# Performance work log

Hardware: AMD Instinct MI355X
Metric: run time of the kernel (lower is better)

## Reference

```python
import jax, jax.numpy as jnp
import numpy as np

N_NODES = 50000
N_EDGES = 800000
IN_F = 128
OUT_F = 64
ALPHA = 0.2  # LeakyReLU negative slope


def setup_inputs() -> dict:
    key = jax.random.key(0)
    k_h, k_e, k_w, k_b, k_a = jax.random.split(key, 5)
    h = jax.random.normal(k_h, (N_NODES, IN_F), dtype=jnp.float32)
    adj = jax.random.randint(k_e, (2, N_EDGES), 0, N_NODES, dtype=jnp.int64)
    # Linear(in_features, out_features): weight [out, in], bias [out]
    W_w = jax.random.normal(k_w, (OUT_F, IN_F), dtype=jnp.float32) * (1.0 / np.sqrt(IN_F))
    W_b = jax.random.normal(k_b, (OUT_F,), dtype=jnp.float32) * 0.01
    a = jax.random.normal(k_a, (1, 2 * OUT_F), dtype=jnp.float32) * (1.0 / np.sqrt(2 * OUT_F))
    return {"h": h, "adj": adj, "W_w": W_w, "W_b": W_b, "a": a}


def reference(h, adj, W_w, W_b, a):
    N = h.shape[0]
    F_out = W_w.shape[0]
    inv_sqrt_f = 1.0 / float(np.sqrt(F_out))

    data = h @ W_w.T + W_b                      # [N, F_out]
    src, dst = adj[0], adj[1]

    # a @ [data[src] || data[dst]]^T  == (data @ a_src)[src] + (data @ a_dst)[dst]
    a_src, a_dst = a[0, :F_out], a[0, F_out:]
    score = (data @ a_src)[src] + (data @ a_dst)[dst]       # [E]
    edge_e = jnp.exp(jax.nn.leaky_relu(score, ALPHA) * inv_sqrt_f)

    # sparse rowsum over source rows (duplicate edges sum, matching COO semantics)
    rowsum = jax.ops.segment_sum(edge_e, src, num_segments=N)  # [N]
    row_zero = rowsum == 0.0
    rowsum = jnp.where(row_zero, 1.0, rowsum)

    # sparse mm: sum_e edge_e * data[dst] into row src; zero rows get a unit self-loop
    h_prime = jax.ops.segment_sum(edge_e[:, None] * data[dst], src, num_segments=N)
    h_prime = h_prime + row_zero[:, None].astype(data.dtype) * data
    return h_prime / rowsum[:, None]
```

## Files before the change

kernel.cpp:

```cpp
#include <hip/hip_runtime.h>
#include <math.h>

#define IN_F 128
#define OUT_F 64
#define ALPHA 0.2f
#define INV_SQRT_F 0.125f
#define CAP 64
#define SUBSH 6
#define SUBSZ 64
#define CAPH 2048
#define HS 136

typedef _Float16 h8  __attribute__((ext_vector_type(8)));
typedef float    f4  __attribute__((ext_vector_type(4)));

__device__ __forceinline__ float edge_w(float sc) {
    float lr = sc > 0.f ? sc : ALPHA * sc;
    return __expf(lr * INV_SQRT_F);
}

__device__ __forceinline__ h8 cvt8(float4 a, float4 b) {
    h8 r;
    r[0] = (_Float16)a.x; r[1] = (_Float16)a.y;
    r[2] = (_Float16)a.z; r[3] = (_Float16)a.w;
    r[4] = (_Float16)b.x; r[5] = (_Float16)b.y;
    r[6] = (_Float16)b.z; r[7] = (_Float16)b.w;
    return r;
}

__global__ __launch_bounds__(256, 4) void k_p1(
    const float* __restrict__ h, const float* __restrict__ W,
    const float* __restrict__ b, const float* __restrict__ a,
    const int* __restrict__ src, const int* __restrict__ dst,
    int* __restrict__ gcur, unsigned* __restrict__ pk,
    _Float16* __restrict__ data_h,
    float* __restrict__ s_src, float* __restrict__ s_dst,
    int n_nodes, int n_edges, int g_p1)
{
    __shared__ _Float16 wsh[OUT_F * HS];
    __shared__ int hist[1024];
    __shared__ int off[1024];
    const int tid = threadIdx.x;

    if ((int)blockIdx.x < g_p1) {
        const int nsub = (n_nodes + SUBSZ - 1) >> SUBSH;
        const int e0 = (int)blockIdx.x * 4096 + tid * 16;

        for (int i = tid; i < nsub; i += 256) hist[i] = 0;
        __syncthreads();

        int s[16], d[16];
        const bool full = (e0 + 16 <= n_edges);
        if (full) {
            #pragma unroll
            for (int c = 0; c < 4; ++c) {
                int4 s4 = *(const int4*)&src[e0 + c * 4];
                int4 d4 = *(const int4*)&dst[e0 + c * 4];
                s[c*4+0] = s4.x; s[c*4+1] = s4.y; s[c*4+2] = s4.z; s[c*4+3] = s4.w;
                d[c*4+0] = d4.x; d[c*4+1] = d4.y; d[c*4+2] = d4.z; d[c*4+3] = d4.w;
            }
            #pragma unroll
            for (int i = 0; i < 16; ++i)
                atomicAdd(&hist[s[i] >> SUBSH], 1);
        } else {
            #pragma unroll
            for (int i = 0; i < 16; ++i) {
                int e = e0 + i;
                s[i] = (e < n_edges) ? src[e] : -1;
                d[i] = (e < n_edges) ? dst[e] : 0;
                if (s[i] >= 0) atomicAdd(&hist[s[i] >> SUBSH], 1);
            }
        }
        __syncthreads();

        for (int i = tid; i < nsub; i += 256) {
            int c = hist[i];
            off[i] = (c > 0) ? atomicAdd(&gcur[i], c) : 0;
            hist[i] = 0;
        }
        __syncthreads();

        #pragma unroll
        for (int i = 0; i < 16; ++i) {
            if (s[i] < 0) continue;
            int sub = s[i] >> SUBSH;
            int r = atomicAdd(&hist[sub], 1);
            int p = off[sub] + r;
            if (p < CAPH)
                pk[(size_t)sub * CAPH + p] =
                    ((unsigned)(s[i] & (SUBSZ - 1)) << 16) | (unsigned)d[i];
        }
        return;
    }

    const int node0 = ((int)blockIdx.x - g_p1) * 64;

    const int wv  = tid >> 6;
    const int lane = tid & 63;
    const int q   = lane >> 4;
    const int col = lane & 15;
    const int r0  = wv * 16;

    const int arow = min(node0 + r0 + col, n_nodes - 1);
    const float* __restrict__ hrow = h + (size_t)arow * IN_F;

    float4 ha[4], hb[4];
    #pragma unroll
    for (int kk = 0; kk < 4; ++kk) {
        const int ko = kk * 32 + q * 8;
        ha[kk] = *(const float4*)&hrow[ko];
        hb[kk] = *(const float4*)&hrow[ko + 4];
    }
    float bb[4], as_[4], ad_[4];
    #pragma unroll
    for (int ct = 0; ct < 4; ++ct) {
        bb[ct]  = b[ct * 16 + col];
        as_[ct] = a[ct * 16 + col];
        ad_[ct] = a[OUT_F + ct * 16 + col];
    }

    for (int i = tid * 8; i < OUT_F * IN_F; i += 2048) {
        int f = i >> 7, k = i & 127;
        float4 va = *(const float4*)&W[i];
        float4 vb = *(const float4*)&W[i + 4];
        *(h8*)&wsh[f * HS + k] = cvt8(va, vb);
    }
    __syncthreads();

    f4 acc[4] = {{0.f,0.f,0.f,0.f},{0.f,0.f,0.f,0.f},
                 {0.f,0.f,0.f,0.f},{0.f,0.f,0.f,0.f}};
    #pragma unroll
    for (int kk = 0; kk < 4; ++kk) {
        const int ko = kk * 32 + q * 8;
        h8 av = cvt8(ha[kk], hb[kk]);
        #pragma unroll
        for (int ct = 0; ct < 4; ++ct) {
            h8 bv = *(const h8*)&wsh[(ct * 16 + col) * HS + ko];
            acc[ct] = __builtin_amdgcn_mfma_f32_16x16x32_f16(av, bv, acc[ct], 0, 0, 0);
        }
    }

    #pragma unroll
    for (int reg = 0; reg < 4; ++reg) {
        int n = node0 + r0 + q * 4 + reg;
        float vv[4], ps = 0.f, pd = 0.f;
        #pragma unroll
        for (int ct = 0; ct < 4; ++ct) {
            float v = acc[ct][reg] + bb[ct];
            vv[ct] = v;
            ps = fmaf(v, as_[ct], ps);
            pd = fmaf(v, ad_[ct], pd);
        }
        #pragma unroll
        for (int m = 1; m <= 8; m <<= 1) {
            ps += __shfl_xor(ps, m, 64);
            pd += __shfl_xor(pd, m, 64);
        }
        if (n < n_nodes) {
            size_t base = (size_t)n * OUT_F + col;
            #pragma unroll
            for (int ct = 0; ct < 4; ++ct)
                data_h[base + ct * 16] = (_Float16)vv[ct];
            if (col == 0) { s_src[n] = ps; s_dst[n] = pd; }
        }
    }
}

__global__ __launch_bounds__(512) void k_bin(
    const unsigned* __restrict__ pk, const int* __restrict__ gcur,
    const float* __restrict__ s_src, const float* __restrict__ s_dst,
    const _Float16* __restrict__ data_h, float* __restrict__ out, int n_nodes)
{
    __shared__ uint2 edl[64 * CAP];
    __shared__ int   lcnt[64];
    __shared__ float ssl[64];
    const int sub  = (int)blockIdx.x;
    const int tid  = threadIdx.x;
    const int nbase = sub * SUBSZ;

    if (tid < 64) {
        lcnt[tid] = 0;
        int n = nbase + tid;
        ssl[tid] = (n < n_nodes) ? s_src[n] : 0.f;
    }
    __syncthreads();

    const int ecnt = min(gcur[sub], CAPH);
    for (int i = tid; i < ecnt; i += 512) {
        unsigned v = pk[(size_t)sub * CAPH + i];
        int s63 = (int)(v >> 16);
        int d = (int)(v & 0xffffu);
        float w = edge_w(ssl[s63] + s_dst[d]);
        int r = atomicAdd(&lcnt[s63], 1);
        if (r < CAP) {
            uint2 e; e.x = (unsigned)d; e.y = __float_as_uint(w);
            edl[s63 * CAP + ((r + 2 * (s63 & 7)) & (CAP - 1))] = e;
        }
    }
    __syncthreads();

    const int wv = tid >> 6, lane = tid & 63;
    const int g  = lane >> 3;
    const int fl = lane & 7;
    const int nl = wv * 8 + g;
    const int n  = nbase + nl;
    const int rot = 2 * (nl & 7);
    const int cn = (n < n_nodes) ? min(lcnt[nl], CAP) : 0;
    const int bbase = nl * CAP;

    float ac[8] = {0.f,0.f,0.f,0.f,0.f,0.f,0.f,0.f};
    float rs = 0.f;
    int t = 0;
    for (; t + 4 <= cn; t += 4) {
        uint2 e0 = edl[bbase + ((t + 0 + rot) & (CAP - 1))];
        uint2 e1 = edl[bbase + ((t + 1 + rot) & (CAP - 1))];
        uint2 e2 = edl[bbase + ((t + 2 + rot) & (CAP - 1))];
        uint2 e3 = edl[bbase + ((t + 3 + rot) & (CAP - 1))];
        h8 x0 = *(const h8*)&data_h[(size_t)e0.x * OUT_F + 8 * fl];
        h8 x1 = *(const h8*)&data_h[(size_t)e1.x * OUT_F + 8 * fl];
        h8 x2 = *(const h8*)&data_h[(size_t)e2.x * OUT_F + 8 * fl];
        h8 x3 = *(const h8*)&data_h[(size_t)e3.x * OUT_F + 8 * fl];
        float w0 = __uint_as_float(e0.y);
        float w1 = __uint_as_float(e1.y);
        float w2 = __uint_as_float(e2.y);
        float w3 = __uint_as_float(e3.y);
        #pragma unroll
        for (int i = 0; i < 8; ++i) ac[i] = fmaf(w0, (float)x0[i], ac[i]);
        #pragma unroll
        for (int i = 0; i < 8; ++i) ac[i] = fmaf(w1, (float)x1[i], ac[i]);
        #pragma unroll
        for (int i = 0; i < 8; ++i) ac[i] = fmaf(w2, (float)x2[i], ac[i]);
        #pragma unroll
        for (int i = 0; i < 8; ++i) ac[i] = fmaf(w3, (float)x3[i], ac[i]);
        rs += (w0 + w1) + (w2 + w3);
    }
    for (; t < cn; ++t) {
        uint2 e0 = edl[bbase + ((t + rot) & (CAP - 1))];
        float w0 = __uint_as_float(e0.y);
        h8 x0 = *(const h8*)&data_h[(size_t)e0.x * OUT_F + 8 * fl];
        #pragma unroll
        for (int i = 0; i < 8; ++i) ac[i] = fmaf(w0, (float)x0[i], ac[i]);
        rs += w0;
    }

    if (n < n_nodes) {
        size_t o = (size_t)n * OUT_F + 8 * fl;
        f4 r0, r1;
        if (rs == 0.f) {
            h8 xv = *(const h8*)&data_h[o];
            r0[0] = (float)xv[0]; r0[1] = (float)xv[1];
            r0[2] = (float)xv[2]; r0[3] = (float)xv[3];
            r1[0] = (float)xv[4]; r1[1] = (float)xv[5];
            r1[2] = (float)xv[6]; r1[3] = (float)xv[7];
        } else {
            float inv = 1.f / rs;
            r0[0] = ac[0] * inv; r0[1] = ac[1] * inv;
            r0[2] = ac[2] * inv; r0[3] = ac[3] * inv;
            r1[0] = ac[4] * inv; r1[1] = ac[5] * inv;
            r1[2] = ac[6] * inv; r1[3] = ac[7] * inv;
        }
        __builtin_nontemporal_store(r0, (f4*)&out[o]);
        __builtin_nontemporal_store(r1, (f4*)&out[o + 4]);
    }
}

extern "C" void kernel_launch(void* const* d_in, const int* in_sizes, int n_in,
                              void* d_out, int out_size, void* d_ws, size_t ws_size,
                              hipStream_t stream)
{
    const float* h   = (const float*)d_in[0];
    const int*   adj = (const int*)  d_in[1];
    const float* W   = (const float*)d_in[2];
    const float* b   = (const float*)d_in[3];
    const float* a   = (const float*)d_in[4];
    float* out = (float*)d_out;

    const int n_nodes = in_sizes[0] / IN_F;
    const int n_edges = in_sizes[1] / 2;
    const int* src = adj;
    const int* dst = adj + n_edges;
    const int nsub = (n_nodes + SUBSZ - 1) >> SUBSH;

    char* p = (char*)d_ws;
    _Float16*       data_h = (_Float16*)p;       p += (size_t)n_nodes * OUT_F * 2;
    unsigned*       pk     = (unsigned*)p;       p += (size_t)nsub * CAPH * 4;
    float*          s_src  = (float*)p;          p += (size_t)n_nodes * 4;
    float*          s_dst  = (float*)p;          p += (size_t)n_nodes * 4;
    int*            gcur   = (int*)p;            p += (size_t)nsub * 4;

    (void)hipMemsetAsync(gcur, 0, (size_t)nsub * sizeof(int), stream);

    const int g_p1  = (n_edges + 4095) / 4096;
    const int g_lin = (n_nodes + 63) / 64;
    k_p1<<<g_p1 + g_lin, 256, 0, stream>>>(
        h, W, b, a, src, dst, gcur, pk, data_h, s_src, s_dst,
        n_nodes, n_edges, g_p1);

    k_bin<<<nsub, 512, 0, stream>>>(
        pk, gcur, s_src, s_dst, data_h, out, n_nodes);
}
```

Measured before the change: 113.6 us.

## Sort nodes by degree within bin for wave balance; use nontemporal edge loads/stores

In the aggregation kernel, the 64 nodes of each bin are ranked by edge count so that each wavefront handles eight nodes of similar degree, which reduces divergence from uneven loop trip counts across lane groups. The edge-index reads, packed-edge writes and packed-edge reads are also made nontemporal to reduce cache pollution for streamed data. The ranking adds a 64x64 compare pass and an extra barrier per block. A few redundant, odd-looking assignments in the zero-row path are harmless.

```diff
diff --git a/kernel.cpp b/kernel.cpp
--- a/kernel.cpp
+++ b/kernel.cpp
@@ -13,6 +13,7 @@
 
 typedef _Float16 h8  __attribute__((ext_vector_type(8)));
 typedef float    f4  __attribute__((ext_vector_type(4)));
+typedef int      i4  __attribute__((ext_vector_type(4)));
 
 __device__ __forceinline__ float edge_w(float sc) {
     float lr = sc > 0.f ? sc : ALPHA * sc;
@@ -54,10 +55,10 @@
         if (full) {
             #pragma unroll
             for (int c = 0; c < 4; ++c) {
-                int4 s4 = *(const int4*)&src[e0 + c * 4];
-                int4 d4 = *(const int4*)&dst[e0 + c * 4];
-                s[c*4+0] = s4.x; s[c*4+1] = s4.y; s[c*4+2] = s4.z; s[c*4+3] = s4.w;
-                d[c*4+0] = d4.x; d[c*4+1] = d4.y; d[c*4+2] = d4.z; d[c*4+3] = d4.w;
+                i4 s4 = __builtin_nontemporal_load((const i4*)&src[e0 + c * 4]);
+                i4 d4 = __builtin_nontemporal_load((const i4*)&dst[e0 + c * 4]);
+                s[c*4+0] = s4[0]; s[c*4+1] = s4[1]; s[c*4+2] = s4[2]; s[c*4+3] = s4[3];
+                d[c*4+0] = d4[0]; d[c*4+1] = d4[1]; d[c*4+2] = d4[2]; d[c*4+3] = d4[3];
             }
             #pragma unroll
             for (int i = 0; i < 16; ++i)
@@ -87,8 +88,9 @@
             int r = atomicAdd(&hist[sub], 1);
             int p = off[sub] + r;
             if (p < CAPH)
-                pk[(size_t)sub * CAPH + p] =
-                    ((unsigned)(s[i] & (SUBSZ - 1)) << 16) | (unsigned)d[i];
+                __builtin_nontemporal_store(
+                    ((unsigned)(s[i] & (SUBSZ - 1)) << 16) | (unsigned)d[i],
+                    &pk[(size_t)sub * CAPH + p]);
         }
         return;
     }
@@ -173,6 +175,7 @@
 {
     __shared__ uint2 edl[64 * CAP];
     __shared__ int   lcnt[64];
+    __shared__ int   nsort[64];
     __shared__ float ssl[64];
     const int sub  = (int)blockIdx.x;
     const int tid  = threadIdx.x;
@@ -187,7 +190,7 @@
 
     const int ecnt = min(gcur[sub], CAPH);
     for (int i = tid; i < ecnt; i += 512) {
-        unsigned v = pk[(size_t)sub * CAPH + i];
+        unsigned v = __builtin_nontemporal_load(&pk[(size_t)sub * CAPH + i]);
         int s63 = (int)(v >> 16);
         int d = (int)(v & 0xffffu);
         float w = edge_w(ssl[s63] + s_dst[d]);
@@ -199,10 +202,22 @@
     }
     __syncthreads();
 
+    if (tid < 64) {
+        int my = lcnt[tid];
+        int r = 0;
+        #pragma unroll 8
+        for (int j = 0; j < 64; ++j) {
+            int dj = lcnt[j];
+            r += (dj > my) || (dj == my && j < tid);
+        }
+        nsort[r] = tid;
+    }
+    __syncthreads();
+
     const int wv = tid >> 6, lane = tid & 63;
     const int g  = lane >> 3;
     const int fl = lane & 7;
-    const int nl = wv * 8 + g;
+    const int nl = nsort[wv * 8 + g];
     const int n  = nbase + nl;
     const int rot = 2 * (nl & 7);
     const int cn = (n < n_nodes) ? min(lcnt[nl], CAP) : 0;
@@ -251,6 +266,8 @@
             r0[0] = (float)xv[0]; r0[1] = (float)xv[1];
             r0[2] = (float)xv[2]; r0[3] = (float)xv[3];
             r1[0] = (float)xv[4]; r1[1] = (float)xv[5];
+            r1[2] = (float)xv[6]; r1[7 - 7] = r1[0];
+            r1[0] = (float)xv[4]; r1[1] = (float)xv[5];
             r1[2] = (float)xv[6]; r1[3] = (float)xv[7];
         } else {
             float inv = 1.f / rs;
```

New measurement: 134.4 us. 18.3% more time.
